# Optimization experiments

Hardware: AMD Instinct MI355X
Metric: run time of the kernel (lower is better)

## Reference

```python
import jax, jax.numpy as jnp
import numpy as np

B, IN, OUT, GRID = 512, 256, 256, 16


def setup_inputs() -> dict:
    key = jax.random.key(0)
    k1, k2, k3 = jax.random.split(key, 3)
    x = jax.random.normal(k1, (B, IN), dtype=jnp.float32)
    # kaiming_uniform_(a=1): gain = sqrt(2/(1+1)) = 1, bound = sqrt(3/fan_in)
    bound = float(np.sqrt(3.0 / IN))
    weights = jax.random.uniform(k2, (OUT, IN), dtype=jnp.float32, minval=-bound, maxval=bound)
    bias = jnp.zeros((OUT,), dtype=jnp.float32)
    # per-edge piecewise-cubic coefficients: (out, in, GRID-1 intervals, 4 coeffs)
    coeffs = 0.1 * jax.random.normal(k3, (OUT, IN, GRID - 1, 4), dtype=jnp.float32)
    return {"x": x, "weights": weights, "bias": bias, "coeffs": coeffs}


def reference(x, weights, bias, coeffs):
    # x: (B, IN); weights: (OUT, IN); coeffs: (OUT, IN, G-1, 4)
    O, I, n_int, _ = coeffs.shape
    G = n_int + 1
    bp = jnp.linspace(-1.0, 1.0, G, dtype=x.dtype)  # shared breakpoint grid
    # weighted per-edge inputs: (B, OUT, IN)
    wx = weights[None, :, :] * x[:, None, :]
    xc = jnp.clip(wx, bp[0], bp[-1])
    idx = jnp.clip(jnp.searchsorted(bp, xc, side="right") - 1, 0, G - 2)  # (B,O,I)
    dx = xc - bp[idx]
    o_ix = jnp.arange(O)[None, :, None]
    i_ix = jnp.arange(I)[None, None, :]
    c = coeffs[o_ix, i_ix, idx]  # gather per-interval coeffs -> (B, O, I, 4)
    # Horner evaluation: c0 + c1*dx + c2*dx^2 + c3*dx^3
    y = ((c[..., 3] * dx + c[..., 2]) * dx + c[..., 1]) * dx + c[..., 0]
    # sum spline outputs over in_features, add bias -> (B, OUT)
    return jnp.sum(y, axis=2) + bias[None, :]
```

## Files before the change

kernel.cpp:

```cpp
#include <hip/hip_runtime.h>

#define B_SZ   512
#define IN_F   256
#define OUT_F  256
#define NINT   15
#define IHALF  128
#define NC4    (IHALF * NINT)

typedef const __attribute__((address_space(1))) void gvoid_t;
typedef __attribute__((address_space(3))) void lvoid_t;

__global__ void xq_kernel(const float* __restrict__ x, float4* __restrict__ xq) {
    int T  = blockIdx.x * 256 + threadIdx.x;
    int b  = T >> 6;
    int i4 = T & 63;
    float4 v = reinterpret_cast<const float4*>(x)[T];
    xq[i4 * 512 + b] = v;
}

__device__ __forceinline__ float kan_eval(float wv, float xv,
                                          const float4* __restrict__ sc, int cbase) {
    const float kD = 2.0f / 15.0f;
    float wx = wv * xv;
    float xc = fminf(fmaxf(wx, -1.0f), 1.0f);
    float u  = __builtin_fmaf(xc, 7.5f, 7.4999f);
    int   i0 = (int)u;
    float f0 = (float)i0;
    float blo = __fadd_rn(__fmul_rn(f0, kD), -1.0f);
    float bhi = __fadd_rn(__fmul_rn(__fadd_rn(f0, 1.0f), kD), -1.0f);
    bool  up = (xc >= bhi);
    int   j  = i0 + (up ? 1 : 0);
    float bj = up ? bhi : blo;
    float dx = xc - bj;
    float4 c = sc[cbase + j];
    return __builtin_fmaf(__builtin_fmaf(__builtin_fmaf(c.w, dx, c.z), dx, c.y), dx, c.x);
}

__global__ __launch_bounds__(512, 4)
void kan_kernel(const float4* __restrict__ xq,
                const float* __restrict__ w,
                const float* __restrict__ bias,
                const float* __restrict__ coeffs,
                float* __restrict__ out)
{
    __shared__ float4 sc[NC4];
    __shared__ float4 sw4[IHALF / 4];

    const int o = blockIdx.x >> 1;
    const int h = blockIdx.x & 1;
    const int b = threadIdx.x;

    const float4* gsrc = reinterpret_cast<const float4*>(coeffs)
                         + ((size_t)o * IN_F + h * IHALF) * NINT;
    #pragma unroll
    for (int k = 0; k < 4; ++k) {
        int t = b + k * 512;
        if (t < NC4) {
            __builtin_amdgcn_global_load_lds((gvoid_t*)(gsrc + t), (lvoid_t*)(sc + t), 16, 0, 0);
        }
    }
    if (b < IHALF / 4) {
        sw4[b] = reinterpret_cast<const float4*>(w + (size_t)o * IN_F + h * IHALF)[b];
    }
    __syncthreads();

    float a0 = 0.f, a1 = 0.f, a2 = 0.f, a3 = 0.f;

    #pragma unroll 4
    for (int i4 = 0; i4 < IHALF / 4; ++i4) {
        float4 xv = xq[(h * 32 + i4) * 512 + b];
        float4 wv = sw4[i4];
        int cb = i4 * 4 * NINT;
        a0 += kan_eval(wv.x, xv.x, sc, cb);
        a1 += kan_eval(wv.y, xv.y, sc, cb + NINT);
        a2 += kan_eval(wv.z, xv.z, sc, cb + 2 * NINT);
        a3 += kan_eval(wv.w, xv.w, sc, cb + 3 * NINT);
    }

    float acc = (a0 + a1) + (a2 + a3);
    if (h == 0) acc += bias[o];
    atomicAdd(out + (size_t)b * OUT_F + o, acc);
}

extern "C" void kernel_launch(void* const* d_in, const int* in_sizes, int n_in,
                              void* d_out, int out_size, void* d_ws, size_t ws_size,
                              hipStream_t stream) {
    (void)ws_size;

    const float *x = nullptr, *wgt = nullptr, *bias = nullptr, *coeffs = nullptr;
    for (int i = 0; i < n_in; ++i) {
        switch (in_sizes[i]) {
            case 512 * 256:           x      = (const float*)d_in[i]; break;
            case 256 * 256:           wgt    = (const float*)d_in[i]; break;
            case 256:                 bias   = (const float*)d_in[i]; break;
            case 256 * 256 * 15 * 4:  coeffs = (const float*)d_in[i]; break;
            default: break;
        }
    }

    float4* xq = (float4*)d_ws;

    hipMemsetAsync(d_out, 0, (size_t)out_size * sizeof(float), stream);
    xq_kernel<<<128, 256, 0, stream>>>(x, xq);
    kan_kernel<<<2 * OUT_F, B_SZ, 0, stream>>>(xq, wgt, bias, coeffs, (float*)d_out);
}
```

Baseline: 40.12 us.

## Add wave-uniform fast path for central spline intervals, fold output zeroing into prep

Before the loop, the coefficients for the three central intervals (6–8) are loaded from LDS as wave-uniform broadcasts. When every lane in a wavefront has w*x inside [bp6, bp9), a ballot selects a branchless select-and-Horner path. Otherwise the wave falls back to the original searchsorted-style per-lane gather. This avoids divergent per-lane LDS gathers, which can bank-conflict, in the common case, at the cost of extra broadcast loads and register pressure. The output memset is also merged into the transpose prep kernel, which removes one launch.

```diff
diff --git a/kernel.cpp b/kernel.cpp
--- a/kernel.cpp
+++ b/kernel.cpp
@@ -10,15 +10,17 @@
 typedef const __attribute__((address_space(1))) void gvoid_t;
 typedef __attribute__((address_space(3))) void lvoid_t;
 
-__global__ void xq_kernel(const float* __restrict__ x, float4* __restrict__ xq) {
-    int T  = blockIdx.x * 256 + threadIdx.x;
-    int b  = T >> 6;
-    int i4 = T & 63;
+__global__ __launch_bounds__(256) void prep_kernel(const float* __restrict__ x,
+                                                   float4* __restrict__ xq,
+                                                   float4* __restrict__ out4) {
+    int T = blockIdx.x * 256 + threadIdx.x;
+    int b = T >> 6, i4 = T & 63;
     float4 v = reinterpret_cast<const float4*>(x)[T];
     xq[i4 * 512 + b] = v;
+    out4[T] = make_float4(0.f, 0.f, 0.f, 0.f);
 }
 
-__device__ __forceinline__ float kan_eval(float wv, float xv,
+__device__ __forceinline__ float kan_slow(float wv, float xv,
                                           const float4* __restrict__ sc, int cbase) {
     const float kD = 2.0f / 15.0f;
     float wx = wv * xv;
@@ -41,7 +43,8 @@
                 const float* __restrict__ w,
                 const float* __restrict__ bias,
                 const float* __restrict__ coeffs,
-                float* __restrict__ out)
+                float* __restrict__ out,
+                float4 bp)
 {
     __shared__ float4 sc[NC4];
     __shared__ float4 sw4[IHALF / 4];
@@ -64,17 +67,45 @@
     }
     __syncthreads();
 
+    const float BP6 = bp.x, BP7 = bp.y, BP8 = bp.z, BP9 = bp.w;
     float a0 = 0.f, a1 = 0.f, a2 = 0.f, a3 = 0.f;
 
-    #pragma unroll 4
+    #pragma unroll 2
     for (int i4 = 0; i4 < IHALF / 4; ++i4) {
+        const float4* crow = sc + i4 * 4 * NINT;
+        float4 c6[4], c7[4], c8[4];
+        #pragma unroll
+        for (int e = 0; e < 4; ++e) {
+            c6[e] = crow[e * NINT + 6];
+            c7[e] = crow[e * NINT + 7];
+            c8[e] = crow[e * NINT + 8];
+        }
+
         float4 xv = xq[(h * 32 + i4) * 512 + b];
         float4 wv = sw4[i4];
-        int cb = i4 * 4 * NINT;
-        a0 += kan_eval(wv.x, xv.x, sc, cb);
-        a1 += kan_eval(wv.y, xv.y, sc, cb + NINT);
-        a2 += kan_eval(wv.z, xv.z, sc, cb + 2 * NINT);
-        a3 += kan_eval(wv.w, xv.w, sc, cb + 3 * NINT);
+        float wvs[4] = {wv.x, wv.y, wv.z, wv.w};
+        float xvs[4] = {xv.x, xv.y, xv.z, xv.w};
+        float ys[4];
+
+        #pragma unroll
+        for (int e = 0; e < 4; ++e) {
+            float wx = wvs[e] * xvs[e];
+            if (__builtin_expect(__ballot(wx < BP6 || wx >= BP9) != 0ull, 0)) {
+                ys[e] = kan_slow(wvs[e], xvs[e], sc, (i4 * 4 + e) * NINT);
+            } else {
+                bool m7 = wx >= BP7, m8 = wx >= BP8;
+                float bj = m8 ? BP8 : (m7 ? BP7 : BP6);
+                float4 t, cc;
+                t.x = m7 ? c7[e].x : c6[e].x;  cc.x = m8 ? c8[e].x : t.x;
+                t.y = m7 ? c7[e].y : c6[e].y;  cc.y = m8 ? c8[e].y : t.y;
+                t.z = m7 ? c7[e].z : c6[e].z;  cc.z = m8 ? c8[e].z : t.z;
+                t.w = m7 ? c7[e].w : c6[e].w;  cc.w = m8 ? c8[e].w : t.w;
+                float dx = wx - bj;
+                ys[e] = __builtin_fmaf(__builtin_fmaf(__builtin_fmaf(
+                            cc.w, dx, cc.z), dx, cc.y), dx, cc.x);
+            }
+        }
+        a0 += ys[0]; a1 += ys[1]; a2 += ys[2]; a3 += ys[3];
     }
 
     float acc = (a0 + a1) + (a2 + a3);
@@ -85,7 +116,7 @@
 extern "C" void kernel_launch(void* const* d_in, const int* in_sizes, int n_in,
                               void* d_out, int out_size, void* d_ws, size_t ws_size,
                               hipStream_t stream) {
-    (void)ws_size;
+    (void)ws_size; (void)out_size;
 
     const float *x = nullptr, *wgt = nullptr, *bias = nullptr, *coeffs = nullptr;
     for (int i = 0; i < n_in; ++i) {
@@ -100,7 +131,14 @@
 
     float4* xq = (float4*)d_ws;
 
-    hipMemsetAsync(d_out, 0, (size_t)out_size * sizeof(float), stream);
-    xq_kernel<<<128, 256, 0, stream>>>(x, xq);
-    kan_kernel<<<2 * OUT_F, B_SZ, 0, stream>>>(xq, wgt, bias, coeffs, (float*)d_out);
+    volatile float kd = 2.0f / 15.0f;
+    float bpv[4];
+    for (int k = 0; k < 4; ++k) {
+        volatile float p = (float)(k + 6) * kd;
+        bpv[k] = p + (-1.0f);
+    }
+    float4 bp = make_float4(bpv[0], bpv[1], bpv[2], bpv[3]);
+
+    prep_kernel<<<128, 256, 0, stream>>>(x, xq, (float4*)d_out);
+    kan_kernel<<<2 * OUT_F, B_SZ, 0, stream>>>(xq, wgt, bias, coeffs, (float*)d_out, bp);
 }
```

Measured after the change: 41.98 us. 4.6% more time.
